# Kernel optimization log

Hardware: AMD Instinct MI355X
Metric: run time of the kernel (lower is better)

The kernel has to match this reference:

```python
import jax, jax.numpy as jnp
import numpy as np

N_NODES = 20000
N_EDGES = 640000
HIDDEN = 256
HEADS = 8
HEAD_DIM = HIDDEN // HEADS
VOCAB = 119
N_FEATS = 9


def setup_inputs() -> dict:
    key = jax.random.key(0)
    ks = jax.random.split(key, 12)
    X = jax.random.randint(ks[0], (N_NODES, N_FEATS), 0, VOCAB)
    edge_row = jnp.sort(jax.random.randint(ks[1], (N_EDGES,), 0, N_NODES))
    edge_col = jax.random.randint(ks[2], (N_EDGES,), 0, N_NODES)
    s = 0.05  # init scale to keep activations sane
    emb_tables = jax.random.normal(ks[3], (N_FEATS, VOCAB, HIDDEN), jnp.float32) * s
    q_w = jax.random.normal(ks[4], (HIDDEN, HIDDEN), jnp.float32) * s
    q_b = jax.random.normal(ks[5], (HIDDEN,), jnp.float32) * s
    k_w = jax.random.normal(ks[6], (HIDDEN, HIDDEN), jnp.float32) * s
    k_b = jax.random.normal(ks[7], (HIDDEN,), jnp.float32) * s
    v_w = jax.random.normal(ks[8], (HIDDEN, HIDDEN), jnp.float32) * s
    v_b = jax.random.normal(ks[9], (HIDDEN,), jnp.float32) * s
    o_w = jax.random.normal(ks[10], (HIDDEN, HIDDEN), jnp.float32) * s
    o_b = jax.random.normal(ks[11], (HIDDEN,), jnp.float32) * s
    return dict(X=X, edge_row=edge_row, edge_col=edge_col, emb_tables=emb_tables,
                q_w=q_w, q_b=q_b, k_w=k_w, k_b=k_b, v_w=v_w, v_b=v_b, o_w=o_w, o_b=o_b)


def reference(X, edge_row, edge_col, emb_tables, q_w, q_b, k_w, k_b, v_w, v_b, o_w, o_b):
    N = X.shape[0]
    # AtomEncoder: sum of per-feature embeddings -> [N, HIDDEN]
    feat_idx = jnp.arange(N_FEATS)[None, :]  # [1, 9]
    h = emb_tables[feat_idx, X].sum(axis=1)  # [N, 9, H] -> [N, H]
    # q/k/v projections (torch Linear: y = x W^T + b), split into heads
    q = (h @ q_w.T + q_b).reshape(N, HEADS, HEAD_DIM) * (HEAD_DIM ** -0.5)
    k = (h @ k_w.T + k_b).reshape(N, HEADS, HEAD_DIM)
    v = (h @ v_w.T + v_b).reshape(N, HEADS, HEAD_DIM)
    # SDDMM: per-edge, per-head scores
    s = jnp.einsum('ehd,ehd->eh', q[edge_row], k[edge_col])  # [E, HEADS]
    # sparse row-wise softmax (over each node's outgoing-edge neighbors)
    m = jax.ops.segment_max(s, edge_row, num_segments=N)
    e = jnp.exp(s - m[edge_row])
    z = jax.ops.segment_sum(e, edge_row, num_segments=N)
    attn = e / z[edge_row]  # [E, HEADS]
    # SPMM: weighted aggregation of neighbor values
    out = jax.ops.segment_sum(attn[:, :, None] * v[edge_col], edge_row, num_segments=N)
    return out.reshape(N, HIDDEN) @ o_w.T + o_b
```

## Files before the change

kernel.cpp:

```cpp
#include <hip/hip_runtime.h>
#include <hip/hip_bf16.h>

#define N_NODES 20000
#define N_EDGES 640000
#define HIDDEN 256
#define HEADS 8
#define HEAD_DIM 32
#define N_FEATS 9
#define VOCAB 119

typedef __hip_bfloat16 bf16;
typedef __attribute__((ext_vector_type(8))) short short8;
typedef __attribute__((ext_vector_type(4))) float f32x4;
typedef __attribute__((ext_vector_type(2))) float f32x2;

__device__ __forceinline__ ushort f2u(float x) { union { ushort u; bf16 b; } c; c.b = __float2bfloat16(x); return c.u; }

__device__ __forceinline__ f32x2 pk_fma(f32x2 a, f32x2 b, f32x2 c) {
    f32x2 d;
    asm("v_pk_fma_f32 %0, %1, %2, %3" : "=v"(d) : "v"(a), "v"(b), "v"(c));
    return d;
}
__device__ __forceinline__ f32x2 pk_add(f32x2 a, f32x2 b) {
    f32x2 d;
    asm("v_pk_add_f32 %0, %1, %2" : "=v"(d) : "v"(a), "v"(b));
    return d;
}

template <int CTRL>
__device__ __forceinline__ float dpp_xor(float v) {
    return __int_as_float(__builtin_amdgcn_update_dpp(
        0, __float_as_int(v), CTRL, 0xf, 0xf, true));
}

__device__ __forceinline__ float fast_exp2(float x) {
#if __has_builtin(__builtin_amdgcn_exp2f)
    return __builtin_amdgcn_exp2f(x);
#else
    return exp2f(x);
#endif
}

#if __has_builtin(__builtin_amdgcn_fdot2_f32_bf16)
typedef __attribute__((ext_vector_type(2))) __bf16 bf16x2_t;
__device__ __forceinline__ float dot2bf(uint a, uint b, float c) {
    return __builtin_amdgcn_fdot2_f32_bf16(__builtin_bit_cast(bf16x2_t, a),
                                           __builtin_bit_cast(bf16x2_t, b), c, false);
}
#else
__device__ __forceinline__ float dot2bf(uint a, uint b, float c) {
    return c + __uint_as_float(a << 16) * __uint_as_float(b << 16)
             + __uint_as_float(a & 0xffff0000u) * __uint_as_float(b & 0xffff0000u);
}
#endif

__global__ void k_pre(const int* __restrict__ X, const float* __restrict__ emb,
                      bf16* __restrict__ h,
                      const float* __restrict__ qw, const float* __restrict__ kw,
                      const float* __restrict__ vw, const float* __restrict__ ow,
                      const float* __restrict__ qb, const float* __restrict__ kb,
                      const float* __restrict__ vb,
                      bf16* __restrict__ wqkv, bf16* __restrict__ wo,
                      float* __restrict__ qkvb,
                      const int* __restrict__ erow, int* __restrict__ row_ptr) {
    int b = blockIdx.x;
    if (b < 5000) {
        int tid = b * 256 + threadIdx.x;
        int n = tid >> 6;
        int c4 = (tid & 63) * 4;
        float4 a = make_float4(0.f, 0.f, 0.f, 0.f);
#pragma unroll
        for (int f = 0; f < N_FEATS; ++f) {
            int idx = X[n * N_FEATS + f];
            float4 e = *(const float4*)(emb + ((size_t)(f * VOCAB + idx)) * HIDDEN + c4);
            a.x += e.x; a.y += e.y; a.z += e.z; a.w += e.w;
        }
        ushort4 o = make_ushort4(f2u(a.x), f2u(a.y), f2u(a.z), f2u(a.w));
        *(ushort4*)((ushort*)h + (size_t)n * HIDDEN + c4) = o;
    } else if (b < 6027) {
        int i = (b - 5000) * 256 + threadIdx.x;
        if (i < 196608) {
            const float* s = i < 65536 ? qw : i < 131072 ? kw : vw;
            wqkv[i] = __float2bfloat16(s[i & 65535]);
        } else if (i < 262144) {
            wo[i - 196608] = __float2bfloat16(ow[i - 196608]);
        } else if (i < 262912) {
            int j = i - 262144;
            const float* s = j < 256 ? qb : j < 512 ? kb : vb;
            qkvb[j] = s[j & 255];
        }
    } else {
        int n = (b - 6027) * 256 + threadIdx.x;
        if (n > N_NODES) return;
        int lo = 0, hi = N_EDGES;
        while (lo < hi) {
            int mid = (lo + hi) >> 1;
            if (erow[mid] < n) lo = mid + 1; else hi = mid;
        }
        row_ptr[n] = lo;
    }
}

template <int MODE, bool GUARD, int TM>
__device__ __forceinline__ void gemm_core(const bf16* __restrict__ A,
                                          const bf16* __restrict__ W,
                                          const float* __restrict__ bias,
                                          void* __restrict__ Y0, void* __restrict__ Y1,
                                          float s_q, int n0, int d0) {
    constexpr int RI = TM / 32;
    __shared__ short As[TM * 72];
    __shared__ short Bs[128 * 72];
    int t = threadIdx.x;
    int lane = t & 63, w = t >> 6;
    int wr = (w >> 1) * (TM / 2), wc = (w & 1) * 64;
    int lr = lane & 15, quad = lane >> 4;

    f32x4 acc[RI][4] = {};
    short8 ra[RI], rb[4];
    int srowA[RI], skoA[RI], srowB[4], skoB[4];
#pragma unroll
    for (int it = 0; it < RI; ++it) { int c = t + 256 * it; srowA[it] = c >> 3; skoA[it] = (c & 7) * 8; }
#pragma unroll
    for (int it = 0; it < 4; ++it) { int c = t + 256 * it; srowB[it] = c >> 3; skoB[it] = (c & 7) * 8; }

#pragma unroll
    for (int it = 0; it < RI; ++it) {
        int n = n0 + srowA[it];
        short8 av = {};
        if (!GUARD || n < N_NODES) av = *(const short8*)(A + (size_t)n * HIDDEN + skoA[it]);
        ra[it] = av;
    }
#pragma unroll
    for (int it = 0; it < 4; ++it)
        rb[it] = *(const short8*)(W + (size_t)(d0 + srowB[it]) * HIDDEN + skoB[it]);
#pragma unroll
    for (int it = 0; it < RI; ++it) *(short8*)(&As[srowA[it] * 72 + skoA[it]]) = ra[it];
#pragma unroll
    for (int it = 0; it < 4; ++it)  *(short8*)(&Bs[srowB[it] * 72 + skoB[it]]) = rb[it];
    __syncthreads();

    for (int k0 = 64; k0 < 256; k0 += 64) {
#pragma unroll
        for (int it = 0; it < RI; ++it) {
            int n = n0 + srowA[it];
            short8 av = {};
            if (!GUARD || n < N_NODES) av = *(const short8*)(A + (size_t)n * HIDDEN + k0 + skoA[it]);
            ra[it] = av;
        }
#pragma unroll
        for (int it = 0; it < 4; ++it)
            rb[it] = *(const short8*)(W + (size_t)(d0 + srowB[it]) * HIDDEN + k0 + skoB[it]);
        {
            short8 af[RI][2], bfr[4][2];
#pragma unroll
            for (int i = 0; i < RI; ++i)
#pragma unroll
                for (int kk = 0; kk < 2; ++kk)
                    af[i][kk] = *(short8*)(&As[(wr + i * 16 + lr) * 72 + kk * 32 + quad * 8]);
#pragma unroll
            for (int j = 0; j < 4; ++j)
#pragma unroll
                for (int kk = 0; kk < 2; ++kk)
                    bfr[j][kk] = *(short8*)(&Bs[(wc + j * 16 + lr) * 72 + kk * 32 + quad * 8]);
#pragma unroll
            for (int kk = 0; kk < 2; ++kk)
#pragma unroll
                for (int i = 0; i < RI; ++i)
#pragma unroll
                    for (int j = 0; j < 4; ++j)
                        acc[i][j] = __builtin_amdgcn_mfma_f32_16x16x32_bf16(
                            af[i][kk], bfr[j][kk], acc[i][j], 0, 0, 0);
        }
        __syncthreads();
#pragma unroll
        for (int it = 0; it < RI; ++it) *(short8*)(&As[srowA[it] * 72 + skoA[it]]) = ra[it];
#pragma unroll
        for (int it = 0; it < 4; ++it)  *(short8*)(&Bs[srowB[it] * 72 + skoB[it]]) = rb[it];
        __syncthreads();
    }
    {
        short8 af[RI][2], bfr[4][2];
#pragma unroll
        for (int i = 0; i < RI; ++i)
#pragma unroll
            for (int kk = 0; kk < 2; ++kk)
                af[i][kk] = *(short8*)(&As[(wr + i * 16 + lr) * 72 + kk * 32 + quad * 8]);
#pragma unroll
        for (int j = 0; j < 4; ++j)
#pragma unroll
            for (int kk = 0; kk < 2; ++kk)
                bfr[j][kk] = *(short8*)(&Bs[(wc + j * 16 + lr) * 72 + kk * 32 + quad * 8]);
#pragma unroll
        for (int kk = 0; kk < 2; ++kk)
#pragma unroll
            for (int i = 0; i < RI; ++i)
#pragma unroll
                for (int j = 0; j < 4; ++j)
                    acc[i][j] = __builtin_amdgcn_mfma_f32_16x16x32_bf16(
                        af[i][kk], bfr[j][kk], acc[i][j], 0, 0, 0);
    }

#pragma unroll
    for (int j = 0; j < 4; ++j) {
        int dbase = d0 + wc + j * 16;
        float bj = bias[dbase + lr];
        if constexpr (MODE == 0) {
            float sc = (dbase < 256) ? s_q : 1.f;
            ushort* dst; int stride;
            if (dbase < 256) {
                dst = (ushort*)Y0 + (size_t)(dbase >> 6) * N_NODES * 64 + (dbase & 63) + lr;
                stride = 64;
            } else if (dbase < 512) {
                int e = dbase - 256;
                dst = (ushort*)Y1 + (size_t)(e >> 6) * N_NODES * 128 + (e & 63) + lr;
                stride = 128;
            } else {
                int e = dbase - 512;
                dst = (ushort*)Y1 + (size_t)(e >> 6) * N_NODES * 128 + 64 + (e & 63) + lr;
                stride = 128;
            }
#pragma unroll
            for (int i = 0; i < RI; ++i)
#pragma unroll
                for (int r = 0; r < 4; ++r) {
                    int n = n0 + wr + i * 16 + quad * 4 + r;
                    if (GUARD && n >= N_NODES) continue;
                    dst[(size_t)n * stride] = f2u((acc[i][j][r] + bj) * sc);
                }
        } else {
            float* dst = (float*)Y0 + dbase + lr;
#pragma unroll
            for (int i = 0; i < RI; ++i)
#pragma unroll
                for (int r = 0; r < 4; ++r) {
                    int n = n0 + wr + i * 16 + quad * 4 + r;
                    if (GUARD && n >= N_NODES) continue;
                    dst[(size_t)n * HIDDEN] = acc[i][j][r] + bj;
                }
        }
    }
}

__global__ __launch_bounds__(256, 2) void k_gemm_qkv(
    const bf16* __restrict__ A, const bf16* __restrict__ wqkv,
    const float* __restrict__ qkvb, ushort* __restrict__ qhp,
    ushort* __restrict__ kvhp, float qscale) {
    int n0 = blockIdx.x * 128;
    if (n0 + 128 <= N_NODES)
        gemm_core<0, false, 128>(A, wqkv, qkvb, qhp, kvhp, qscale, n0, blockIdx.y * 128);
    else
        gemm_core<0, true, 128>(A, wqkv, qkvb, qhp, kvhp, qscale, n0, blockIdx.y * 128);
}

__global__ __launch_bounds__(256, 4) void k_gemm_o(
    const bf16* __restrict__ A, const bf16* __restrict__ W,
    const float* __restrict__ bias, float* __restrict__ Y) {
    int n0 = blockIdx.x * 64;
    if (n0 + 64 <= N_NODES)
        gemm_core<1, false, 64>(A, W, bias, Y, nullptr, 1.f, n0, blockIdx.y * 128);
    else
        gemm_core<1, true, 64>(A, W, bias, Y, nullptr, 1.f, n0, blockIdx.y * 128);
}

__global__ __launch_bounds__(256) void k_attn(
    const int* __restrict__ row_ptr, const int* __restrict__ col,
    const ushort* __restrict__ qhp, const ushort* __restrict__ kvhp,
    bf16* __restrict__ agg) {
    int b = blockIdx.x;
    int x = b & 7;
    int hp = x & 3;
    int wave = threadIdx.x >> 6;
    int n = (b >> 3) * 8 + (x >> 2) * 4 + wave;
    int lane = threadIdx.x & 63;
    int my = lane >> 3;
    int d8 = lane & 7;

    int start = row_ptr[n];
    int deg = row_ptr[n + 1] - start;

    ushort* orow = (ushort*)agg + (size_t)n * HIDDEN + hp * 64;
    if (deg == 0) {
        if (lane < 8) { uint4 zo = {}; *(uint4*)(orow + lane * 8) = zo; }
        return;
    }

    const ushort* qrow = qhp + ((size_t)hp * N_NODES + n) * 64;
    uint4 qu = *(const uint4*)(qrow + d8 * 8);

    const ushort* kvbase = kvhp + (size_t)hp * N_NODES * 128;
    const int* cb = col + start;
    int degm = deg - my;

    float z = 0.f;
    f32x2 av0 = {0.f, 0.f}, av1 = {0.f, 0.f}, av2v = {0.f, 0.f}, av3 = {0.f, 0.f};

#define ATTN_COMPUTE(K, V, IT8) do {                                                      \
        float sa_ = dot2bf((K).x, qu.x, 0.f);                                             \
        float sb_ = dot2bf((K).y, qu.y, 0.f);                                             \
        sa_ = dot2bf((K).z, qu.z, sa_);                                                   \
        sb_ = dot2bf((K).w, qu.w, sb_);                                                   \
        float s_ = sa_ + sb_;                                                             \
        s_ += dpp_xor<0xB1>(s_);                                                          \
        s_ += dpp_xor<0x4E>(s_);                                                          \
        float p_ = ((IT8) < degm) ? fast_exp2(s_) : 0.f;                                  \
        z += p_;                                                                          \
        f32x2 pp_; pp_.x = p_; pp_.y = p_;                                                \
        f32x2 vf0_, vf1_, vf2_, vf3_;                                                     \
        vf0_.x = __uint_as_float((V).x << 16); vf0_.y = __uint_as_float((V).x & 0xffff0000u); \
        vf1_.x = __uint_as_float((V).y << 16); vf1_.y = __uint_as_float((V).y & 0xffff0000u); \
        vf2_.x = __uint_as_float((V).z << 16); vf2_.y = __uint_as_float((V).z & 0xffff0000u); \
        vf3_.x = __uint_as_float((V).w << 16); vf3_.y = __uint_as_float((V).w & 0xffff0000u); \
        av0  = pk_fma(vf0_, pp_, av0);                                                    \
        av1  = pk_fma(vf1_, pp_, av1);                                                    \
        av2v = pk_fma(vf2_, pp_, av2v);                                                   \
        av3  = pk_fma(vf3_, pp_, av3);                                                    \
    } while (0)

    if (deg <= 64) {
        int c_all = cb[min(lane, deg - 1)];
        int nb = (deg + 7) >> 3;
        int np = nb >> 1;

        int c0 = __shfl(c_all, my);
        int c1 = __shfl(c_all, (8 + my) & 63);
        uint o0 = ((uint)c0 << 7) + (uint)d8 * 8;
        uint o1 = ((uint)c1 << 7) + (uint)d8 * 8;
        uint4 ka  = *(const uint4*)(kvbase + o0), va  = *(const uint4*)(kvbase + o0 + 64);
        uint4 kb2 = *(const uint4*)(kvbase + o1), vb2 = *(const uint4*)(kvbase + o1 + 64);

#pragma unroll 1
        for (int pit = 0; pit < np; ++pit) {
            int it = pit * 2;
            uint4 kn0, vn0, kn1, vn1;
            bool pf = (pit + 1 < np) || (nb & 1);
            if (pf) {
                int cn0 = __shfl(c_all, ((it + 2) * 8 + my) & 63);
                int cn1 = __shfl(c_all, ((it + 3) * 8 + my) & 63);
                uint on0 = ((uint)cn0 << 7) + (uint)d8 * 8;
                uint on1 = ((uint)cn1 << 7) + (uint)d8 * 8;
                kn0 = *(const uint4*)(kvbase + on0); vn0 = *(const uint4*)(kvbase + on0 + 64);
                kn1 = *(const uint4*)(kvbase + on1); vn1 = *(const uint4*)(kvbase + on1 + 64);
            }
            ATTN_COMPUTE(ka, va, it * 8);
            ATTN_COMPUTE(kb2, vb2, it * 8 + 8);
            if (pf) { ka = kn0; va = vn0; kb2 = kn1; vb2 = vn1; }
        }
        if (nb & 1)
            ATTN_COMPUTE(ka, va, (nb - 1) * 8);
    } else {
        for (int i = 0; i < deg; i += 8) {
            int idx = i + my;
            int cidx = idx < deg ? idx : deg - 1;
            int c = cb[cidx];
            uint off = ((uint)c << 7) + (uint)d8 * 8;
            uint4 ku = *(const uint4*)(kvbase + off);
            uint4 vu = *(const uint4*)(kvbase + off + 64);
            ATTN_COMPUTE(ku, vu, i);
        }
    }
#undef ATTN_COMPUTE

    z += dpp_xor<0x128>(z);
    z += __shfl_xor(z, 16);
    z += __shfl_xor(z, 32);

    bool b3 = (lane & 8) != 0, b4 = (lane & 16) != 0, b5 = (lane & 32) != 0;
    f32x2 sd0 = b3 ? av0 : av2v;
    f32x2 sd1 = b3 ? av1 : av3;
    f32x2 r0, r1;
    r0.x = dpp_xor<0x128>(sd0.x); r0.y = dpp_xor<0x128>(sd0.y);
    r1.x = dpp_xor<0x128>(sd1.x); r1.y = dpp_xor<0x128>(sd1.y);
    f32x2 t0 = pk_add(b3 ? av2v : av0, r0);
    f32x2 t1 = pk_add(b3 ? av3  : av1, r1);
    f32x2 sdu = b4 ? t0 : t1;
    f32x2 ru; ru.x = __shfl_xor(sdu.x, 16); ru.y = __shfl_xor(sdu.y, 16);
    f32x2 u = pk_add(b4 ? t1 : t0, ru);
    float sw = b5 ? u.x : u.y;
    float rw = __shfl_xor(sw, 32);
    float w = (b5 ? u.y : u.x) + rw;

    int dim = d8 * 8 + ((lane >> 3) & 1) * 4 + ((lane >> 4) & 1) * 2 + ((lane >> 5) & 1);
    float invz = 1.f / z;
    orow[dim] = f2u(w * invz);
}

extern "C" void kernel_launch(void* const* d_in, const int* in_sizes, int n_in,
                              void* d_out, int out_size, void* d_ws, size_t ws_size,
                              hipStream_t stream) {
    const int*   X    = (const int*)d_in[0];
    const int*   erow = (const int*)d_in[1];
    const int*   ecol = (const int*)d_in[2];
    const float* emb  = (const float*)d_in[3];
    const float* q_w  = (const float*)d_in[4];
    const float* q_b  = (const float*)d_in[5];
    const float* k_w  = (const float*)d_in[6];
    const float* k_b  = (const float*)d_in[7];
    const float* v_w  = (const float*)d_in[8];
    const float* v_b  = (const float*)d_in[9];
    const float* o_w  = (const float*)d_in[10];
    const float* o_b  = (const float*)d_in[11];
    float* out = (float*)d_out;

    char* ws = (char*)d_ws;
    bf16*   h    = (bf16*)(ws);
    bf16*   agg  = (bf16*)(ws);
    ushort* qhp  = (ushort*)(ws + 10240000);
    ushort* kvhp = (ushort*)(ws + 20480000);
    bf16*   wqkv = (bf16*)(ws + 40960000);
    bf16*   wo   = (bf16*)(ws + 41353216);
    float*  qkvb = (float*)(ws + 41484288);
    int* row_ptr = (int*)(ws + 41487360);

    k_pre<<<6106, 256, 0, stream>>>(X, emb, h, q_w, k_w, v_w, o_w,
                                    q_b, k_b, v_b, wqkv, wo, qkvb, erow, row_ptr);

    const float qscale = 0.25503486121587466f;
    dim3 gqkv((N_NODES + 127) / 128, 768 / 128);
    k_gemm_qkv<<<gqkv, 256, 0, stream>>>(h, wqkv, qkvb, qhp, kvhp, qscale);

    k_attn<<<N_NODES, 256, 0, stream>>>(row_ptr, ecol, qhp, kvhp, agg);

    dim3 go((N_NODES + 63) / 64, HIDDEN / 128);
    k_gemm_o<<<go, 256, 0, stream>>>(agg, wo, o_b, out);
}
```

Baseline: 177.9 us.

## Restructure attention kernel: per-edge score lanes with fully unrolled gather for small degrees

Rewrites the attention kernel so that for degree ≤32 each pair of lanes computes one edge score (two halves of the 64-dim head-pair), and for degree ≤64 each lane owns one edge and computes both head scores, replacing the old 8-lane cooperative dot products plus DPP reductions. All K and V rows are gathered up front with full unrolling, so many loads are in flight at once instead of a two-deep software pipeline. Adds launch bounds of 4 blocks per CU and makes the wave index scalar. The unrolled path uses more registers, and each lane now reads a full 64-element query row.

```diff
diff --git a/kernel.cpp b/kernel.cpp
--- a/kernel.cpp
+++ b/kernel.cpp
@@ -262,108 +262,28 @@
         gemm_core<1, true, 64>(A, W, bias, Y, nullptr, 1.f, n0, blockIdx.y * 128);
 }
 
-__global__ __launch_bounds__(256) void k_attn(
-    const int* __restrict__ row_ptr, const int* __restrict__ col,
-    const ushort* __restrict__ qhp, const ushort* __restrict__ kvhp,
-    bf16* __restrict__ agg) {
-    int b = blockIdx.x;
-    int x = b & 7;
-    int hp = x & 3;
-    int wave = threadIdx.x >> 6;
-    int n = (b >> 3) * 8 + (x >> 2) * 4 + wave;
-    int lane = threadIdx.x & 63;
-    int my = lane >> 3;
-    int d8 = lane & 7;
-
-    int start = row_ptr[n];
-    int deg = row_ptr[n + 1] - start;
-
-    ushort* orow = (ushort*)agg + (size_t)n * HIDDEN + hp * 64;
-    if (deg == 0) {
-        if (lane < 8) { uint4 zo = {}; *(uint4*)(orow + lane * 8) = zo; }
-        return;
-    }
-
-    const ushort* qrow = qhp + ((size_t)hp * N_NODES + n) * 64;
-    uint4 qu = *(const uint4*)(qrow + d8 * 8);
-
-    const ushort* kvbase = kvhp + (size_t)hp * N_NODES * 128;
-    const int* cb = col + start;
-    int degm = deg - my;
-
-    float z = 0.f;
-    f32x2 av0 = {0.f, 0.f}, av1 = {0.f, 0.f}, av2v = {0.f, 0.f}, av3 = {0.f, 0.f};
-
-#define ATTN_COMPUTE(K, V, IT8) do {                                                      \
-        float sa_ = dot2bf((K).x, qu.x, 0.f);                                             \
-        float sb_ = dot2bf((K).y, qu.y, 0.f);                                             \
-        sa_ = dot2bf((K).z, qu.z, sa_);                                                   \
-        sb_ = dot2bf((K).w, qu.w, sb_);                                                   \
-        float s_ = sa_ + sb_;                                                             \
-        s_ += dpp_xor<0xB1>(s_);                                                          \
-        s_ += dpp_xor<0x4E>(s_);                                                          \
-        float p_ = ((IT8) < degm) ? fast_exp2(s_) : 0.f;                                  \
-        z += p_;                                                                          \
-        f32x2 pp_; pp_.x = p_; pp_.y = p_;                                                \
-        f32x2 vf0_, vf1_, vf2_, vf3_;                                                     \
-        vf0_.x = __uint_as_float((V).x << 16); vf0_.y = __uint_as_float((V).x & 0xffff0000u); \
-        vf1_.x = __uint_as_float((V).y << 16); vf1_.y = __uint_as_float((V).y & 0xffff0000u); \
-        vf2_.x = __uint_as_float((V).z << 16); vf2_.y = __uint_as_float((V).z & 0xffff0000u); \
-        vf3_.x = __uint_as_float((V).w << 16); vf3_.y = __uint_as_float((V).w & 0xffff0000u); \
-        av0  = pk_fma(vf0_, pp_, av0);                                                    \
-        av1  = pk_fma(vf1_, pp_, av1);                                                    \
-        av2v = pk_fma(vf2_, pp_, av2v);                                                   \
-        av3  = pk_fma(vf3_, pp_, av3);                                                    \
-    } while (0)
-
-    if (deg <= 64) {
-        int c_all = cb[min(lane, deg - 1)];
-        int nb = (deg + 7) >> 3;
-        int np = nb >> 1;
-
-        int c0 = __shfl(c_all, my);
-        int c1 = __shfl(c_all, (8 + my) & 63);
-        uint o0 = ((uint)c0 << 7) + (uint)d8 * 8;
-        uint o1 = ((uint)c1 << 7) + (uint)d8 * 8;
-        uint4 ka  = *(const uint4*)(kvbase + o0), va  = *(const uint4*)(kvbase + o0 + 64);
-        uint4 kb2 = *(const uint4*)(kvbase + o1), vb2 = *(const uint4*)(kvbase + o1 + 64);
-
-#pragma unroll 1
-        for (int pit = 0; pit < np; ++pit) {
-            int it = pit * 2;
-            uint4 kn0, vn0, kn1, vn1;
-            bool pf = (pit + 1 < np) || (nb & 1);
-            if (pf) {
-                int cn0 = __shfl(c_all, ((it + 2) * 8 + my) & 63);
-                int cn1 = __shfl(c_all, ((it + 3) * 8 + my) & 63);
-                uint on0 = ((uint)cn0 << 7) + (uint)d8 * 8;
-                uint on1 = ((uint)cn1 << 7) + (uint)d8 * 8;
-                kn0 = *(const uint4*)(kvbase + on0); vn0 = *(const uint4*)(kvbase + on0 + 64);
-                kn1 = *(const uint4*)(kvbase + on1); vn1 = *(const uint4*)(kvbase + on1 + 64);
-            }
-            ATTN_COMPUTE(ka, va, it * 8);
-            ATTN_COMPUTE(kb2, vb2, it * 8 + 8);
-            if (pf) { ka = kn0; va = vn0; kb2 = kn1; vb2 = vn1; }
-        }
-        if (nb & 1)
-            ATTN_COMPUTE(ka, va, (nb - 1) * 8);
-    } else {
-        for (int i = 0; i < deg; i += 8) {
-            int idx = i + my;
-            int cidx = idx < deg ? idx : deg - 1;
-            int c = cb[cidx];
-            uint off = ((uint)c << 7) + (uint)d8 * 8;
-            uint4 ku = *(const uint4*)(kvbase + off);
-            uint4 vu = *(const uint4*)(kvbase + off + 64);
-            ATTN_COMPUTE(ku, vu, i);
-        }
-    }
-#undef ATTN_COMPUTE
-
-    z += dpp_xor<0x128>(z);
-    z += __shfl_xor(z, 16);
-    z += __shfl_xor(z, 32);
-
+
+template <int NIT>
+__device__ __forceinline__ void pv_accum(const uint4* vv, const float* pb,
+                                         f32x2& av0, f32x2& av1, f32x2& av2v, f32x2& av3) {
+#pragma unroll
+    for (int it = 0; it < NIT; ++it) {
+        f32x2 pp; pp.x = pb[it]; pp.y = pb[it];
+        f32x2 vf0, vf1, vf2, vf3;
+        vf0.x = __uint_as_float(vv[it].x << 16); vf0.y = __uint_as_float(vv[it].x & 0xffff0000u);
+        vf1.x = __uint_as_float(vv[it].y << 16); vf1.y = __uint_as_float(vv[it].y & 0xffff0000u);
+        vf2.x = __uint_as_float(vv[it].z << 16); vf2.y = __uint_as_float(vv[it].z & 0xffff0000u);
+        vf3.x = __uint_as_float(vv[it].w << 16); vf3.y = __uint_as_float(vv[it].w & 0xffff0000u);
+        av0  = pk_fma(vf0, pp, av0);
+        av1  = pk_fma(vf1, pp, av1);
+        av2v = pk_fma(vf2, pp, av2v);
+        av3  = pk_fma(vf3, pp, av3);
+    }
+}
+
+__device__ __forceinline__ void attn_combine(int lane, int d8, float z,
+                                             f32x2 av0, f32x2 av1, f32x2 av2v, f32x2 av3,
+                                             ushort* __restrict__ orow) {
     bool b3 = (lane & 8) != 0, b4 = (lane & 16) != 0, b5 = (lane & 32) != 0;
     f32x2 sd0 = b3 ? av0 : av2v;
     f32x2 sd1 = b3 ? av1 : av3;
@@ -378,10 +298,189 @@
     float sw = b5 ? u.x : u.y;
     float rw = __shfl_xor(sw, 32);
     float w = (b5 ? u.y : u.x) + rw;
-
     int dim = d8 * 8 + ((lane >> 3) & 1) * 4 + ((lane >> 4) & 1) * 2 + ((lane >> 5) & 1);
-    float invz = 1.f / z;
-    orow[dim] = f2u(w * invz);
+    orow[dim] = f2u(w * (1.f / z));
+}
+
+__global__ __launch_bounds__(256, 4) void k_attn(
+    const int* __restrict__ row_ptr, const int* __restrict__ col,
+    const ushort* __restrict__ qhp, const ushort* __restrict__ kvhp,
+    bf16* __restrict__ agg) {
+    int b = blockIdx.x;
+    int x = b & 7;
+    int hp = x & 3;
+    int wave = __builtin_amdgcn_readfirstlane((int)(threadIdx.x >> 6));
+    int n = (b >> 3) * 8 + (x >> 2) * 4 + wave;
+    int lane = threadIdx.x & 63;
+    int my = lane >> 3;
+    int d8 = lane & 7;
+
+    int start = row_ptr[n];
+    int deg = row_ptr[n + 1] - start;
+
+    ushort* orow = (ushort*)agg + (size_t)n * HIDDEN + hp * 64;
+    if (deg == 0) {
+        if (lane < 8) { uint4 zo = {}; *(uint4*)(orow + lane * 8) = zo; }
+        return;
+    }
+
+    const ushort* qrow = qhp + ((size_t)hp * N_NODES + n) * 64;
+    const ushort* kvbase = kvhp + (size_t)hp * N_NODES * 128;
+    const int* cb = col + start;
+
+    if (deg <= 32) {
+        int e = lane >> 1, h = lane & 1;
+        int c_e = cb[min(e, deg - 1)];
+        const ushort* kp = kvbase + (((size_t)(uint)c_e) << 7) + (uint)h * 32;
+        const ushort* qp = qrow + (uint)h * 32;
+
+        int cv[4]; uint4 vv[4];
+#pragma unroll
+        for (int it = 0; it < 4; ++it) cv[it] = __shfl(c_e, (it * 8 + my) * 2);
+#pragma unroll
+        for (int it = 0; it < 4; ++it)
+            vv[it] = *(const uint4*)(kvbase + (((size_t)(uint)cv[it]) << 7) + 64 + (uint)d8 * 8);
+
+        uint4 kk[4], qq[4];
+#pragma unroll
+        for (int i = 0; i < 4; ++i) kk[i] = *(const uint4*)(kp + i * 8);
+#pragma unroll
+        for (int i = 0; i < 4; ++i) qq[i] = *(const uint4*)(qp + i * 8);
+
+        float c0 = dot2bf(kk[0].x, qq[0].x, 0.f);
+        float c1 = dot2bf(kk[0].y, qq[0].y, 0.f);
+        float c2 = dot2bf(kk[0].z, qq[0].z, 0.f);
+        float c3 = dot2bf(kk[0].w, qq[0].w, 0.f);
+#pragma unroll
+        for (int i = 1; i < 4; ++i) {
+            c0 = dot2bf(kk[i].x, qq[i].x, c0);
+            c1 = dot2bf(kk[i].y, qq[i].y, c1);
+            c2 = dot2bf(kk[i].z, qq[i].z, c2);
+            c3 = dot2bf(kk[i].w, qq[i].w, c3);
+        }
+        float s = (c0 + c1) + (c2 + c3);
+        float p = (e < deg) ? fast_exp2(s) : 0.f;
+
+        float z = p;
+        z += dpp_xor<0x4E>(z);
+        z += dpp_xor<0x124>(z);
+        z += dpp_xor<0x128>(z);
+        z += __shfl_xor(z, 16);
+        z += __shfl_xor(z, 32);
+        float zo = __shfl_xor(z, 1);
+        float zf = (h == (d8 >> 2)) ? z : zo;
+
+        float pb[4];
+#pragma unroll
+        for (int it = 0; it < 4; ++it)
+            pb[it] = __shfl(p, (it * 8 + my) * 2 + (d8 >> 2));
+
+        f32x2 av0 = {0.f, 0.f}, av1 = {0.f, 0.f}, av2v = {0.f, 0.f}, av3 = {0.f, 0.f};
+        pv_accum<4>(vv, pb, av0, av1, av2v, av3);
+        attn_combine(lane, d8, zf, av0, av1, av2v, av3, orow);
+
+    } else if (deg <= 64) {
+        int c_all = cb[min(lane, deg - 1)];
+        const ushort* kp = kvbase + (((size_t)(uint)c_all) << 7);
+
+        int cv[8]; uint4 vv[8];
+#pragma unroll
+        for (int it = 0; it < 8; ++it) cv[it] = __shfl(c_all, it * 8 + my);
+#pragma unroll
+        for (int it = 0; it < 8; ++it)
+            vv[it] = *(const uint4*)(kvbase + (((size_t)(uint)cv[it]) << 7) + 64 + (uint)d8 * 8);
+
+        uint4 kk[8], qv[8];
+#pragma unroll
+        for (int i = 0; i < 8; ++i) kk[i] = *(const uint4*)(kp + i * 8);
+#pragma unroll
+        for (int i = 0; i < 8; ++i) qv[i] = *(const uint4*)(qrow + i * 8);
+
+        float a0 = dot2bf(kk[0].x, qv[0].x, 0.f);
+        float a1 = dot2bf(kk[0].y, qv[0].y, 0.f);
+        float a2 = dot2bf(kk[0].z, qv[0].z, 0.f);
+        float a3 = dot2bf(kk[0].w, qv[0].w, 0.f);
+        float b0 = dot2bf(kk[4].x, qv[4].x, 0.f);
+        float b1 = dot2bf(kk[4].y, qv[4].y, 0.f);
+        float b2 = dot2bf(kk[4].z, qv[4].z, 0.f);
+        float b3s = dot2bf(kk[4].w, qv[4].w, 0.f);
+#pragma unroll
+        for (int i = 1; i < 4; ++i) {
+            a0 = dot2bf(kk[i].x, qv[i].x, a0);
+            a1 = dot2bf(kk[i].y, qv[i].y, a1);
+            a2 = dot2bf(kk[i].z, qv[i].z, a2);
+            a3 = dot2bf(kk[i].w, qv[i].w, a3);
+            b0 = dot2bf(kk[4 + i].x, qv[4 + i].x, b0);
+            b1 = dot2bf(kk[4 + i].y, qv[4 + i].y, b1);
+            b2 = dot2bf(kk[4 + i].z, qv[4 + i].z, b2);
+            b3s = dot2bf(kk[4 + i].w, qv[4 + i].w, b3s);
+        }
+        float sA = (a0 + a1) + (a2 + a3);
+        float sB = (b0 + b1) + (b2 + b3s);
+        bool val = lane < deg;
+        float pA = val ? fast_exp2(sA) : 0.f;
+        float pB = val ? fast_exp2(sB) : 0.f;
+
+        f32x2 zz; zz.x = pA; zz.y = pB;
+        {
+            f32x2 r;
+            r.x = dpp_xor<0xB1>(zz.x);  r.y = dpp_xor<0xB1>(zz.y);  zz = pk_add(zz, r);
+            r.x = dpp_xor<0x4E>(zz.x);  r.y = dpp_xor<0x4E>(zz.y);  zz = pk_add(zz, r);
+            r.x = dpp_xor<0x124>(zz.x); r.y = dpp_xor<0x124>(zz.y); zz = pk_add(zz, r);
+            r.x = dpp_xor<0x128>(zz.x); r.y = dpp_xor<0x128>(zz.y); zz = pk_add(zz, r);
+            r.x = __shfl_xor(zz.x, 16); r.y = __shfl_xor(zz.y, 16); zz = pk_add(zz, r);
+            r.x = __shfl_xor(zz.x, 32); r.y = __shfl_xor(zz.y, 32); zz = pk_add(zz, r);
+        }
+        float zf = (d8 < 4) ? zz.x : zz.y;
+
+        bool hB = (d8 >= 4);
+        float pb[8];
+#pragma unroll
+        for (int it = 0; it < 8; ++it) {
+            float pa_ = __shfl(pA, it * 8 + my);
+            float pb_ = __shfl(pB, it * 8 + my);
+            pb[it] = hB ? pb_ : pa_;
+        }
+
+        f32x2 av0 = {0.f, 0.f}, av1 = {0.f, 0.f}, av2v = {0.f, 0.f}, av3 = {0.f, 0.f};
+        pv_accum<8>(vv, pb, av0, av1, av2v, av3);
+        attn_combine(lane, d8, zf, av0, av1, av2v, av3, orow);
+
+    } else {
+        uint4 qu = *(const uint4*)(qrow + d8 * 8);
+        float z = 0.f;
+        f32x2 av0 = {0.f, 0.f}, av1 = {0.f, 0.f}, av2v = {0.f, 0.f}, av3 = {0.f, 0.f};
+        for (int i = 0; i < deg; i += 8) {
+            int idx = i + my;
+            int cidx = idx < deg ? idx : deg - 1;
+            int c = cb[cidx];
+            const ushort* kp = kvbase + (((size_t)(uint)c) << 7) + (uint)d8 * 8;
+            uint4 ku = *(const uint4*)(kp);
+            uint4 vu = *(const uint4*)(kp + 64);
+            float s = dot2bf(ku.x, qu.x, 0.f);
+            s = dot2bf(ku.y, qu.y, s);
+            s = dot2bf(ku.z, qu.z, s);
+            s = dot2bf(ku.w, qu.w, s);
+            s += dpp_xor<0xB1>(s);
+            s += dpp_xor<0x4E>(s);
+            float p = (idx < deg) ? fast_exp2(s) : 0.f;
+            z += p;
+            f32x2 pp; pp.x = p; pp.y = p;
+            f32x2 vf0, vf1, vf2, vf3;
+            vf0.x = __uint_as_float(vu.x << 16); vf0.y = __uint_as_float(vu.x & 0xffff0000u);
+            vf1.x = __uint_as_float(vu.y << 16); vf1.y = __uint_as_float(vu.y & 0xffff0000u);
+            vf2.x = __uint_as_float(vu.z << 16); vf2.y = __uint_as_float(vu.z & 0xffff0000u);
+            vf3.x = __uint_as_float(vu.w << 16); vf3.y = __uint_as_float(vu.w & 0xffff0000u);
+            av0  = pk_fma(vf0, pp, av0);
+            av1  = pk_fma(vf1, pp, av1);
+            av2v = pk_fma(vf2, pp, av2v);
+            av3  = pk_fma(vf3, pp, av3);
+        }
+        z += dpp_xor<0x128>(z);
+        z += __shfl_xor(z, 16);
+        z += __shfl_xor(z, 32);
+        attn_combine(lane, d8, z, av0, av1, av2v, av3, orow);
+    }
 }
 
 extern "C" void kernel_launch(void* const* d_in, const int* in_sizes, int n_in,
```

New measurement: 190.0 us. 6.8% more time.
